# Kernel optimization log

Hardware: AMD Instinct MI355X
Metric: run time of the kernel (lower is better)

Reference implementation:

```python
import jax, jax.numpy as jnp
import numpy as np

B, S, D, H, ADJ = 32, 512, 512, 8, 512
HD = D // H  # 64
NEG_SLOPE = 0.2


def layer_norm(x, g, b, eps=1e-5):
    m = jnp.mean(x, axis=-1, keepdims=True)
    v = jnp.var(x, axis=-1, keepdims=True)
    return (x - m) / jnp.sqrt(v + eps) * g + b


def setup_inputs() -> dict:
    key = jax.random.key(0)
    ks = jax.random.split(key, 8)
    def n(k, shape, s=0.02):
        return jax.random.normal(k, shape, dtype=jnp.float32) * s
    return {
        'x': jax.random.normal(ks[0], (B, S, D), dtype=jnp.float32),
        'adj': jax.random.normal(ks[1], (B, S, ADJ), dtype=jnp.float32),
        'w_W': n(ks[2], (D, D)), 'w_b': jnp.zeros((D,), jnp.float32),
        'a_w': n(ks[3], (2 * HD,)),
        'sem_W': n(ks[4], (D, ADJ)), 'sem_b': jnp.zeros((D,), jnp.float32),
        'ff1_W': n(ks[5], (2 * D, D)), 'ff1_b': jnp.zeros((2 * D,), jnp.float32),
        'ff2_W': n(ks[6], (D, 2 * D)), 'ff2_b': jnp.zeros((D,), jnp.float32),
        'ln1_g': jnp.ones((D,), jnp.float32), 'ln1_b': jnp.zeros((D,), jnp.float32),
        'ln2_g': jnp.ones((D,), jnp.float32), 'ln2_b': jnp.zeros((D,), jnp.float32),
    }


def reference(x, adj, w_W, w_b, a_w, sem_W, sem_b, ff1_W, ff1_b, ff2_W, ff2_b,
              ln1_g, ln1_b, ln2_g, ln2_b):
    residual = x
    # semantic adjacency: Linear(adj_dim -> out_dim) then softmax; out_dim == S
    adj_s = jax.nn.softmax(adj @ sem_W.T + sem_b, axis=-1)  # (B, S, S)

    # GATConv: projection + additive attention.
    # a([h_i, h_j]) == a_src . h_i + a_dst . h_j  (linear, no bias), so the
    # O(S^2 * 2*hd) concat of the original is replaced by a broadcast-add
    # of two per-node scores — identical math.
    h = (x @ w_W.T + w_b).reshape(B, S, H, HD).transpose(0, 2, 1, 3)  # (B,H,S,hd)
    a_src, a_dst = a_w[:HD], a_w[HD:]
    src = jnp.einsum('bhsd,d->bhs', h, a_src)  # score contribution of node i
    dst = jnp.einsum('bhsd,d->bhs', h, a_dst)  # score contribution of node j
    e = jax.nn.leaky_relu(src[:, :, :, None] + dst[:, :, None, :], NEG_SLOPE)
    e = jnp.where(adj_s[:, None, :, :] == 0, -1e9, e)  # masked_fill(adj==0)
    attn = jax.nn.softmax(e, axis=-1)  # (B, H, S, S)
    out = jnp.einsum('bhij,bhjd->bhid', attn, h)  # weighted aggregate
    out = out.transpose(0, 2, 1, 3).reshape(B, S, D)

    out = layer_norm(out + residual, ln1_g, ln1_b)
    residual2 = out
    ff = jax.nn.gelu(out @ ff1_W.T + ff1_b, approximate=False) @ ff2_W.T + ff2_b
    return layer_norm(ff + residual2, ln2_g, ln2_b)
```

## Files before the change

kernel.cpp:

```cpp
#include <hip/hip_runtime.h>
#include <cstdint>
#include <cstddef>


typedef __bf16 bfx8 __attribute__((ext_vector_type(8)));
typedef float v4f __attribute__((ext_vector_type(4)));
typedef unsigned short u16x8 __attribute__((ext_vector_type(8)));

__device__ __forceinline__ float bf2f(unsigned short h) {
    unsigned int u = ((unsigned int)h) << 16;
    return __builtin_bit_cast(float, u);
}
__device__ __forceinline__ unsigned short f2bf(float x) {
    unsigned int u = __builtin_bit_cast(unsigned int, x);
    unsigned int r = (u + 0x7fffu + ((u >> 16) & 1u)) >> 16;
    return (unsigned short)r;
}
__device__ __forceinline__ u16x8 load8cvt(const float* p) {
    float4 a = *(const float4*)p;
    float4 b = *(const float4*)(p + 4);
    u16x8 r;
    r[0] = f2bf(a.x); r[1] = f2bf(a.y); r[2] = f2bf(a.z); r[3] = f2bf(a.w);
    r[4] = f2bf(b.x); r[5] = f2bf(b.y); r[6] = f2bf(b.z); r[7] = f2bf(b.w);
    return r;
}
__device__ __forceinline__ void gl_lds16(const unsigned short* g, unsigned short* l) {
    __builtin_amdgcn_global_load_lds((const __attribute__((address_space(1))) void*)g,
                                     (__attribute__((address_space(3))) void*)l, 16, 0, 0);
}

__global__ __launch_bounds__(256) void cvt_kernel(const float* __restrict__ in,
                                                  unsigned short* __restrict__ out) {
    const int id = blockIdx.x * 256 + threadIdx.x;
    *(u16x8*)(out + (size_t)id * 8) = load8cvt(in + (size_t)id * 8);
}

#define BM 128
#define BN 128
#define BK 64

template <int EPI, typename CT>
__global__ __launch_bounds__(256, 4) void gemm_bt(
    const unsigned short* __restrict__ A, const unsigned short* __restrict__ Bw,
    const float* __restrict__ bias, CT* __restrict__ C,
    int M, int N, int K) {
    __shared__ unsigned short sA[BM * BK];
    __shared__ unsigned short sB[BN * BK];
    const int t = threadIdx.x;
    const int lane = t & 63;
    const int w = t >> 6;
    const int wm = w >> 1, wn = w & 1;
    const int m0 = blockIdx.x * BM, n0 = blockIdx.y * BN;
    const int mrow = lane & 15, kq = lane >> 4;

    v4f acc[4][4];
#pragma unroll
    for (int i = 0; i < 4; i++)
#pragma unroll
        for (int j = 0; j < 4; j++) acc[i][j] = (v4f)(0.0f);

    const int sr = t >> 3;
    const int sc = ((t & 7) ^ (sr & 7)) * 8;
    const unsigned short* pA[4];
    const unsigned short* pB[4];
#pragma unroll
    for (int c = 0; c < 4; c++) {
        pA[c] = A + (size_t)(m0 + c * 32 + sr) * K + sc;
        pB[c] = Bw + (size_t)(n0 + c * 32 + sr) * K + sc;
    }

    for (int k0 = 0; k0 < K; k0 += BK) {
#pragma unroll
        for (int c = 0; c < 4; c++) {
            gl_lds16(pA[c] + k0, &sA[(c * 256 + t) * 8]);
            gl_lds16(pB[c] + k0, &sB[(c * 256 + t) * 8]);
        }
        __syncthreads();
#pragma unroll
        for (int kh = 0; kh < 2; kh++) {
            bfx8 af[4], bfr[4];
#pragma unroll
            for (int mi = 0; mi < 4; mi++) {
                const int r = wm * 64 + mi * 16 + mrow;
                const int ch = (kh * 4 + kq) ^ (mrow & 7);
                af[mi] = __builtin_bit_cast(bfx8, *(const u16x8*)&sA[r * BK + ch * 8]);
            }
#pragma unroll
            for (int ni = 0; ni < 4; ni++) {
                const int r = wn * 64 + ni * 16 + mrow;
                const int ch = (kh * 4 + kq) ^ (mrow & 7);
                bfr[ni] = __builtin_bit_cast(bfx8, *(const u16x8*)&sB[r * BK + ch * 8]);
            }
#pragma unroll
            for (int mi = 0; mi < 4; mi++)
#pragma unroll
                for (int ni = 0; ni < 4; ni++)
                    acc[mi][ni] = __builtin_amdgcn_mfma_f32_16x16x32_bf16(af[mi], bfr[ni], acc[mi][ni], 0, 0, 0);
        }
        __syncthreads();
    }
#pragma unroll
    for (int ni = 0; ni < 4; ni++) {
        const int col = n0 + wn * 64 + ni * 16 + mrow;
        const float bv = bias[col];
#pragma unroll
        for (int mi = 0; mi < 4; mi++) {
#pragma unroll
            for (int r = 0; r < 4; r++) {
                const int row = m0 + wm * 64 + mi * 16 + kq * 4 + r;
                float val = acc[mi][ni][r] + bv;
                if (EPI == 1) val = 0.5f * val * (1.0f + erff(val * 0.70710678118654752f));
                if constexpr (__is_same(CT, float)) C[(size_t)row * N + col] = val;
                else C[(size_t)row * N + col] = f2bf(val);
            }
        }
    }
}

__global__ __launch_bounds__(256) void srcdst_kernel(
    const unsigned short* __restrict__ hbuf, const float* __restrict__ aw,
    float* __restrict__ src, float* __restrict__ dst) {
    const int id = blockIdx.x * 256 + threadIdx.x;
    const int i = id & 511;
    const int bh = id >> 9;
    const int head = bh & 7, b = bh >> 3;
    const unsigned short* hp = hbuf + ((size_t)(b * 512 + i)) * 512 + head * 64;
    float s = 0.f, d = 0.f;
#pragma unroll
    for (int c = 0; c < 8; c++) {
        u16x8 hv = *(const u16x8*)(hp + c * 8);
        float4 a0 = *(const float4*)(aw + c * 8);
        float4 a1 = *(const float4*)(aw + c * 8 + 4);
        float4 d0 = *(const float4*)(aw + 64 + c * 8);
        float4 d1 = *(const float4*)(aw + 64 + c * 8 + 4);
        float av[8] = {a0.x, a0.y, a0.z, a0.w, a1.x, a1.y, a1.z, a1.w};
        float dv[8] = {d0.x, d0.y, d0.z, d0.w, d1.x, d1.y, d1.z, d1.w};
#pragma unroll
        for (int j = 0; j < 8; j++) {
            float x = bf2f(hv[j]);
            s += x * av[j];
            d += x * dv[j];
        }
    }
    src[id] = s;
    dst[id] = d;
}

__global__ __launch_bounds__(256, 2) void attn_kernel(
    const unsigned short* __restrict__ hbuf, const float* __restrict__ srcg,
    const float* __restrict__ dstg, unsigned short* __restrict__ aout) {
    __shared__ unsigned short Ht[64 * 512];

    const int t = threadIdx.x, lane = t & 63, w = t >> 6;
    const int bh = blockIdx.x, b = bh >> 3, head = bh & 7;
    const size_t hbase = (size_t)(b * 512) * 512 + head * 64;

    {
        const int d = lane;
        const int sw = d & 7;
#pragma unroll
        for (int jc = 0; jc < 16; ++jc) {
            const int j0 = w * 128 + jc * 8;
            u16x8 pack;
#pragma unroll
            for (int jj = 0; jj < 8; jj++)
                pack[jj] = hbuf[hbase + (size_t)(j0 + jj) * 512 + d];
            const int gj = (j0 >> 3) ^ sw;
            *(u16x8*)&Ht[d * 512 + gj * 8] = pack;
        }
    }
    __syncthreads();

    float dmax = -1e30f;
#pragma unroll
    for (int q = 0; q < 8; q++) dmax = fmaxf(dmax, dstg[bh * 512 + q * 64 + lane]);
#pragma unroll
    for (int off = 32; off >= 1; off >>= 1) dmax = fmaxf(dmax, __shfl_xor(dmax, off, 64));

    const int mrow = lane & 15, kq = lane >> 4;

#pragma unroll 1
    for (int g = 0; g < 8; ++g) {
        const int ibase = w * 128 + g * 16;
        const float si = srcg[bh * 512 + ibase + mrow];
        const float e0 = si + dmax;
        const float mi = e0 > 0.f ? e0 : 0.2f * e0;
        float sum = 0.f;
        v4f acc[4];
#pragma unroll
        for (int nt = 0; nt < 4; nt++) acc[nt] = (v4f)(0.0f);

#pragma unroll 2
        for (int ks = 0; ks < 16; ++ks) {
            const int j0 = ks * 32 + kq * 8;
            float4 d0 = *(const float4*)&dstg[bh * 512 + j0];
            float4 d1 = *(const float4*)&dstg[bh * 512 + j0 + 4];
            float dj[8] = {d0.x, d0.y, d0.z, d0.w, d1.x, d1.y, d1.z, d1.w};
            u16x8 au;
#pragma unroll
            for (int jj = 0; jj < 8; jj++) {
                float e = si + dj[jj];
                e = e > 0.f ? e : 0.2f * e;
                float p = __expf(e - mi);
                sum += p;
                au[jj] = f2bf(p);
            }
            bfx8 af = __builtin_bit_cast(bfx8, au);
#pragma unroll
            for (int nt = 0; nt < 4; nt++) {
                const int dd = nt * 16 + mrow;
                const int gj = (ks * 4 + kq) ^ (dd & 7);
                bfx8 bfrag = __builtin_bit_cast(bfx8, *(const u16x8*)&Ht[dd * 512 + gj * 8]);
                acc[nt] = __builtin_amdgcn_mfma_f32_16x16x32_bf16(af, bfrag, acc[nt], 0, 0, 0);
            }
        }
        sum += __shfl_xor(sum, 16, 64);
        sum += __shfl_xor(sum, 32, 64);
#pragma unroll
        for (int r = 0; r < 4; r++) {
            const float rs = __shfl(sum, kq * 4 + r, 64);
            const float inv = 1.0f / rs;
            const int row = b * 512 + ibase + kq * 4 + r;
#pragma unroll
            for (int nt = 0; nt < 4; nt++) {
                const int col = head * 64 + nt * 16 + mrow;
                aout[(size_t)row * 512 + col] = f2bf(acc[nt][r] * inv);
            }
        }
    }
}

template <typename T>
__device__ __forceinline__ void loadf8(const T* p, float* v) {
    if constexpr (__is_same(T, float)) {
        float4 a = *(const float4*)p;
        float4 b = *(const float4*)(p + 4);
        v[0] = a.x; v[1] = a.y; v[2] = a.z; v[3] = a.w;
        v[4] = b.x; v[5] = b.y; v[6] = b.z; v[7] = b.w;
    } else {
        u16x8 h = *(const u16x8*)p;
#pragma unroll
        for (int j = 0; j < 8; j++) v[j] = bf2f(h[j]);
    }
}

template <typename XT, typename RT, typename OT>
__global__ __launch_bounds__(256) void ln_kernel(
    const XT* __restrict__ xin, const RT* __restrict__ res,
    const float* __restrict__ gg, const float* __restrict__ bb,
    OT* __restrict__ out) {
    const int row = blockIdx.x * 4 + (threadIdx.x >> 6);
    const int lane = threadIdx.x & 63;
    const size_t base = (size_t)row * 512 + lane * 8;
    float xv[8], rv[8], v[8];
    loadf8(xin + base, xv);
    loadf8(res + base, rv);
    float s1 = 0.f, s2 = 0.f;
#pragma unroll
    for (int j = 0; j < 8; j++) {
        v[j] = xv[j] + rv[j];
        s1 += v[j];
        s2 += v[j] * v[j];
    }
#pragma unroll
    for (int off = 1; off < 64; off <<= 1) {
        s1 += __shfl_xor(s1, off, 64);
        s2 += __shfl_xor(s2, off, 64);
    }
    const float mean = s1 * (1.0f / 512.0f);
    const float var = s2 * (1.0f / 512.0f) - mean * mean;
    const float rstd = rsqrtf(var + 1e-5f);
    float gv[8], bv[8];
    loadf8(gg + lane * 8, gv);
    loadf8(bb + lane * 8, bv);
    float o[8];
#pragma unroll
    for (int j = 0; j < 8; j++) o[j] = (v[j] - mean) * rstd * gv[j] + bv[j];
    if constexpr (__is_same(OT, float)) {
        *(float4*)(out + base) = make_float4(o[0], o[1], o[2], o[3]);
        *(float4*)(out + base + 4) = make_float4(o[4], o[5], o[6], o[7]);
    } else {
        u16x8 ov;
#pragma unroll
        for (int j = 0; j < 8; j++) ov[j] = f2bf(o[j]);
        *(u16x8*)(out + base) = ov;
    }
}

extern "C" void kernel_launch(void* const* d_in, const int* in_sizes, int n_in,
                              void* d_out, int out_size, void* d_ws, size_t ws_size,
                              hipStream_t stream) {
    const float* x   = (const float*)d_in[0];
    const float* wW  = (const float*)d_in[2];
    const float* wb  = (const float*)d_in[3];
    const float* aw  = (const float*)d_in[4];
    const float* f1W = (const float*)d_in[7];
    const float* f1b = (const float*)d_in[8];
    const float* f2W = (const float*)d_in[9];
    const float* f2b = (const float*)d_in[10];
    const float* g1  = (const float*)d_in[11];
    const float* b1  = (const float*)d_in[12];
    const float* g2  = (const float*)d_in[13];
    const float* b2  = (const float*)d_in[14];
    float* out = (float*)d_out;

    char* ws = (char*)d_ws;
    unsigned short* xb    = (unsigned short*)(ws);
    unsigned short* hb    = (unsigned short*)(ws + 16777216);
    unsigned short* aoutb = (unsigned short*)(ws);
    unsigned short* gbuf  = (unsigned short*)(ws + 16777216);
    unsigned short* y     = (unsigned short*)(ws);
    float* src            = (float*)(ws + 50331648);
    float* dst            = (float*)(ws + 50331648 + 524288);
    unsigned short* wWb   = (unsigned short*)(ws + 52428800);
    unsigned short* f1Wb  = (unsigned short*)(ws + 53477376);
    unsigned short* f2Wb  = (unsigned short*)(ws + 55574528);

    (void)in_sizes; (void)n_in; (void)out_size; (void)ws_size;

    dim3 blk(256);
    cvt_kernel<<<dim3(4096), blk, 0, stream>>>(x, xb);
    cvt_kernel<<<dim3(128), blk, 0, stream>>>(wW, wWb);
    cvt_kernel<<<dim3(256), blk, 0, stream>>>(f1W, f1Wb);
    cvt_kernel<<<dim3(256), blk, 0, stream>>>(f2W, f2Wb);
    gemm_bt<0, unsigned short><<<dim3(128, 4), blk, 0, stream>>>(xb, wWb, wb, hb, 16384, 512, 512);
    srcdst_kernel<<<dim3(512), blk, 0, stream>>>(hb, aw, src, dst);
    attn_kernel<<<dim3(256), blk, 0, stream>>>(hb, src, dst, aoutb);
    ln_kernel<unsigned short, float, unsigned short>
        <<<dim3(4096), blk, 0, stream>>>(aoutb, x, g1, b1, y);
    gemm_bt<1, unsigned short><<<dim3(128, 8), blk, 0, stream>>>(y, f1Wb, f1b, gbuf, 16384, 1024, 512);
    gemm_bt<0, float><<<dim3(128, 4), blk, 0, stream>>>(gbuf, f2Wb, f2b, out, 16384, 512, 1024);
    ln_kernel<float, unsigned short, float>
        <<<dim3(4096), blk, 0, stream>>>(out, y, g2, b2, out);
}
```

Baseline: 277.4 us.

## Split attention rows across two 512-thread blocks and read bf16 residual in LN1

The attention kernel now launches 512 blocks of 512 threads, with each (batch, head) pair split into two halves of query rows. Each wave processes two 16-row groups at once and shares the LDS B-fragments between the two MFMA chains, which raises parallelism and B reuse. The workspace layout is changed so the bf16 copy of x stays live, and LN1 reads that bf16 residual instead of fp32 x, which cuts memory traffic but lowers residual precision. Each block still transposes the full 64x512 H slice into LDS, so the H load is duplicated across the two halves.

```diff
diff --git a/kernel.cpp b/kernel.cpp
--- a/kernel.cpp
+++ b/kernel.cpp
@@ -146,21 +146,23 @@
     dst[id] = d;
 }
 
-__global__ __launch_bounds__(256, 2) void attn_kernel(
+__global__ __launch_bounds__(512, 4) void attn_kernel(
     const unsigned short* __restrict__ hbuf, const float* __restrict__ srcg,
     const float* __restrict__ dstg, unsigned short* __restrict__ aout) {
     __shared__ unsigned short Ht[64 * 512];
 
     const int t = threadIdx.x, lane = t & 63, w = t >> 6;
-    const int bh = blockIdx.x, b = bh >> 3, head = bh & 7;
+    const int bq = blockIdx.x;
+    const int bh = bq >> 1, half = bq & 1;
+    const int b = bh >> 3, head = bh & 7;
     const size_t hbase = (size_t)(b * 512) * 512 + head * 64;
 
     {
         const int d = lane;
         const int sw = d & 7;
 #pragma unroll
-        for (int jc = 0; jc < 16; ++jc) {
-            const int j0 = w * 128 + jc * 8;
+        for (int jc = 0; jc < 8; ++jc) {
+            const int j0 = w * 64 + jc * 8;
             u16x8 pack;
 #pragma unroll
             for (int jj = 0; jj < 8; jj++)
@@ -178,54 +180,67 @@
     for (int off = 32; off >= 1; off >>= 1) dmax = fmaxf(dmax, __shfl_xor(dmax, off, 64));
 
     const int mrow = lane & 15, kq = lane >> 4;
-
-#pragma unroll 1
-    for (int g = 0; g < 8; ++g) {
-        const int ibase = w * 128 + g * 16;
-        const float si = srcg[bh * 512 + ibase + mrow];
-        const float e0 = si + dmax;
-        const float mi = e0 > 0.f ? e0 : 0.2f * e0;
-        float sum = 0.f;
-        v4f acc[4];
-#pragma unroll
-        for (int nt = 0; nt < 4; nt++) acc[nt] = (v4f)(0.0f);
+    const int rbase = half * 256 + w * 32;
+
+    const float si0 = srcg[bh * 512 + rbase + mrow];
+    const float si1 = srcg[bh * 512 + rbase + 16 + mrow];
+    const float e00 = si0 + dmax, e01 = si1 + dmax;
+    const float mi0 = fmaxf(e00, 0.2f * e00);
+    const float mi1 = fmaxf(e01, 0.2f * e01);
+
+    float sum0 = 0.f, sum1 = 0.f;
+    v4f acc0[4], acc1[4];
+#pragma unroll
+    for (int nt = 0; nt < 4; nt++) { acc0[nt] = (v4f)(0.0f); acc1[nt] = (v4f)(0.0f); }
 
 #pragma unroll 2
-        for (int ks = 0; ks < 16; ++ks) {
-            const int j0 = ks * 32 + kq * 8;
-            float4 d0 = *(const float4*)&dstg[bh * 512 + j0];
-            float4 d1 = *(const float4*)&dstg[bh * 512 + j0 + 4];
-            float dj[8] = {d0.x, d0.y, d0.z, d0.w, d1.x, d1.y, d1.z, d1.w};
-            u16x8 au;
-#pragma unroll
-            for (int jj = 0; jj < 8; jj++) {
-                float e = si + dj[jj];
-                e = e > 0.f ? e : 0.2f * e;
-                float p = __expf(e - mi);
-                sum += p;
-                au[jj] = f2bf(p);
-            }
-            bfx8 af = __builtin_bit_cast(bfx8, au);
-#pragma unroll
-            for (int nt = 0; nt < 4; nt++) {
-                const int dd = nt * 16 + mrow;
-                const int gj = (ks * 4 + kq) ^ (dd & 7);
-                bfx8 bfrag = __builtin_bit_cast(bfx8, *(const u16x8*)&Ht[dd * 512 + gj * 8]);
-                acc[nt] = __builtin_amdgcn_mfma_f32_16x16x32_bf16(af, bfrag, acc[nt], 0, 0, 0);
-            }
-        }
-        sum += __shfl_xor(sum, 16, 64);
-        sum += __shfl_xor(sum, 32, 64);
-#pragma unroll
-        for (int r = 0; r < 4; r++) {
-            const float rs = __shfl(sum, kq * 4 + r, 64);
-            const float inv = 1.0f / rs;
-            const int row = b * 512 + ibase + kq * 4 + r;
-#pragma unroll
-            for (int nt = 0; nt < 4; nt++) {
-                const int col = head * 64 + nt * 16 + mrow;
-                aout[(size_t)row * 512 + col] = f2bf(acc[nt][r] * inv);
-            }
+    for (int ks = 0; ks < 16; ++ks) {
+        const int j0 = ks * 32 + kq * 8;
+        float4 d0 = *(const float4*)&dstg[bh * 512 + j0];
+        float4 d1 = *(const float4*)&dstg[bh * 512 + j0 + 4];
+        float dj[8] = {d0.x, d0.y, d0.z, d0.w, d1.x, d1.y, d1.z, d1.w};
+        bfx8 bfr[4];
+#pragma unroll
+        for (int nt = 0; nt < 4; nt++) {
+            const int dd = nt * 16 + mrow;
+            const int gj = (ks * 4 + kq) ^ (dd & 7);
+            bfr[nt] = __builtin_bit_cast(bfx8, *(const u16x8*)&Ht[dd * 512 + gj * 8]);
+        }
+        bfx8 a0, a1;
+#pragma unroll
+        for (int jj = 0; jj < 8; jj++) {
+            const float t0 = si0 + dj[jj];
+            const float l0 = fmaxf(t0, 0.2f * t0);
+            const float p0 = __expf(l0 - mi0);
+            sum0 += p0;
+            a0[jj] = (__bf16)p0;
+            const float t1 = si1 + dj[jj];
+            const float l1 = fmaxf(t1, 0.2f * t1);
+            const float p1 = __expf(l1 - mi1);
+            sum1 += p1;
+            a1[jj] = (__bf16)p1;
+        }
+#pragma unroll
+        for (int nt = 0; nt < 4; nt++) {
+            acc0[nt] = __builtin_amdgcn_mfma_f32_16x16x32_bf16(a0, bfr[nt], acc0[nt], 0, 0, 0);
+            acc1[nt] = __builtin_amdgcn_mfma_f32_16x16x32_bf16(a1, bfr[nt], acc1[nt], 0, 0, 0);
+        }
+    }
+    sum0 += __shfl_xor(sum0, 16, 64);
+    sum0 += __shfl_xor(sum0, 32, 64);
+    sum1 += __shfl_xor(sum1, 16, 64);
+    sum1 += __shfl_xor(sum1, 32, 64);
+#pragma unroll
+    for (int r = 0; r < 4; r++) {
+        const float inv0 = 1.0f / __shfl(sum0, kq * 4 + r, 64);
+        const float inv1 = 1.0f / __shfl(sum1, kq * 4 + r, 64);
+        const int row0 = b * 512 + rbase + kq * 4 + r;
+        const int row1 = row0 + 16;
+#pragma unroll
+        for (int nt = 0; nt < 4; nt++) {
+            const int col = head * 64 + nt * 16 + mrow;
+            aout[(size_t)row0 * 512 + col] = f2bf(acc0[nt][r] * inv0);
+            aout[(size_t)row1 * 512 + col] = f2bf(acc1[nt][r] * inv1);
         }
     }
 }
@@ -307,9 +322,9 @@
     char* ws = (char*)d_ws;
     unsigned short* xb    = (unsigned short*)(ws);
     unsigned short* hb    = (unsigned short*)(ws + 16777216);
-    unsigned short* aoutb = (unsigned short*)(ws);
-    unsigned short* gbuf  = (unsigned short*)(ws + 16777216);
-    unsigned short* y     = (unsigned short*)(ws);
+    unsigned short* aoutb = (unsigned short*)(ws + 33554432);
+    unsigned short* y     = (unsigned short*)(ws + 33554432);
+    unsigned short* gbuf  = (unsigned short*)(ws);
     float* src            = (float*)(ws + 50331648);
     float* dst            = (float*)(ws + 50331648 + 524288);
     unsigned short* wWb   = (unsigned short*)(ws + 52428800);
@@ -325,9 +340,9 @@
     cvt_kernel<<<dim3(256), blk, 0, stream>>>(f2W, f2Wb);
     gemm_bt<0, unsigned short><<<dim3(128, 4), blk, 0, stream>>>(xb, wWb, wb, hb, 16384, 512, 512);
     srcdst_kernel<<<dim3(512), blk, 0, stream>>>(hb, aw, src, dst);
-    attn_kernel<<<dim3(256), blk, 0, stream>>>(hb, src, dst, aoutb);
-    ln_kernel<unsigned short, float, unsigned short>
-        <<<dim3(4096), blk, 0, stream>>>(aoutb, x, g1, b1, y);
+    attn_kernel<<<dim3(512), dim3(512), 0, stream>>>(hb, src, dst, aoutb);
+    ln_kernel<unsigned short, unsigned short, unsigned short>
+        <<<dim3(4096), blk, 0, stream>>>(aoutb, xb, g1, b1, y);
     gemm_bt<1, unsigned short><<<dim3(128, 8), blk, 0, stream>>>(y, f1Wb, f1b, gbuf, 16384, 1024, 512);
     gemm_bt<0, float><<<dim3(128, 4), blk, 0, stream>>>(gbuf, f2Wb, f2b, out, 16384, 512, 1024);
     ln_kernel<float, unsigned short, float>
```

After: 249.6 us. 10.0% less time.
